# Kernel tuning notes

Measured on AMD Instinct MI355X. Metric: run time of the kernel, lower is better.

Reference implementation:

```python
import jax, jax.numpy as jnp
import numpy as np

F_DIM = 128; HID = 32; C = 8 * HID; DEPTH = 5; K = 3; HEADS = 8
JK_H = (7 * C) // 2  # 896, PyG JumpingKnowledge('lstm', C, jk_depth=7)
FLEX = 512; CLASSES = 10; GATE_H = 21 * HID
BS = 512; NPG = 23; N_NODES = BS * NPG
EPS = 1e-5


def _bn(x, gamma=None, beta=None):
    # training-mode BatchNorm1d (biased variance), affine optional
    mu = x.mean(0)
    var = x.var(0)
    y = (x - mu) * jax.lax.rsqrt(var + EPS)
    return y * gamma + beta if gamma is not None else y


def _lstm(seq, w_ih, w_hh, b_ih, b_hh):
    # seq: [T, N, C] -> hidden states [T, N, H]; torch gate order i,f,g,o
    n = seq.shape[1]
    hdim = w_hh.shape[1]
    def step(carry, xt):
        h, c = carry
        z = xt @ w_ih.T + h @ w_hh.T + b_ih + b_hh
        i, f, g, o = jnp.split(z, 4, axis=-1)
        c = jax.nn.sigmoid(f) * c + jax.nn.sigmoid(i) * jnp.tanh(g)
        h = jax.nn.sigmoid(o) * jnp.tanh(c)
        return (h, c), h
    init = (jnp.zeros((n, hdim), seq.dtype), jnp.zeros((n, hdim), seq.dtype))
    _, hs = jax.lax.scan(step, init, seq)
    return hs


def _forward(x, conv1_w, conv1_b, bn1_g, bn1_b, ll1_w, ll1_b, tag_w, tag_b,
             gat_w, gat_asrc, gat_adst, gat_b,
             lw_ih_f, lw_hh_f, lb_ih_f, lb_hh_f, lw_ih_b, lw_hh_b, lb_ih_b, lb_hh_b,
             jk_w, jk_b, fff_w1, fff_b1, fff_w2, fff_b2,
             gate_w1, gate_b1, gate_w2, gate_b2,
             conv2_w, conv2_b, bn2_g, bn2_b, fc_w, fc_b,
             edge_index, batch, num_graphs):
    n, f = x.shape
    bs = num_graphs
    # --- temporal preprocessing: PE over node axis (d_model=23), Conv1d, BN ---
    xt = x.reshape(bs, NPG, f).transpose(0, 2, 1)            # [bs, F, 23]
    pos = jnp.arange(f, dtype=x.dtype)[:, None]
    div = jnp.exp(jnp.arange(0, NPG, 2, dtype=x.dtype) * (-np.log(10000.0) / NPG))
    pe = jnp.zeros((f, NPG), x.dtype)
    pe = pe.at[:, 0::2].set(jnp.sin(pos * div))
    pe = pe.at[:, 1::2].set(jnp.cos(pos * div)[:, :(NPG - 1) // 2])
    xt = (xt + pe[None]).transpose(0, 2, 1)                  # [bs, 23, F]
    xt = jax.lax.conv_general_dilated(xt, conv1_w, (1,), [(1, 1)],
            dimension_numbers=('NCH', 'OIH', 'NCH')) + conv1_b[None, :, None]
    h = _bn(xt.reshape(n, f), bn1_g, bn1_b) @ ll1_w + ll1_b  # [N, HID]
    # --- symmetric gcn_norm (no self loops) shared by all TAGConv layers ---
    src, dst = edge_index[0], edge_index[1]
    deg = jax.ops.segment_sum(jnp.ones(src.shape, h.dtype), dst, n)
    dinv = jnp.where(deg > 0, jax.lax.rsqrt(jnp.maximum(deg, 1.0)), 0.0)
    wnorm = dinv[src] * dinv[dst]                            # [E]
    # GAT uses self loops
    loop = jnp.arange(n, dtype=src.dtype)
    src_sl = jnp.concatenate([src, loop])
    dst_sl = jnp.concatenate([dst, loop])

    jk_seq = []
    for i in range(DEPTH):
        # TAGConv: concat powers of normalized adjacency, then linear
        xs = h
        feats = [h]
        for _ in range(K):
            xs = jax.ops.segment_sum(wnorm[:, None] * xs[src], dst, n)
            feats.append(xs)
        tag = jnp.concatenate(feats, axis=-1) @ tag_w[i] + tag_b[i]
        h = _bn(h + tag)                                     # SublayerConnection (BN affine=False)
        # GATConv, heads=8, concat
        g = (h @ gat_w[i]).reshape(n, HEADS, HID)
        a = jax.nn.leaky_relu((g * gat_asrc[i]).sum(-1)[src_sl]
                              + (g * gat_adst[i]).sum(-1)[dst_sl], 0.2)  # [E', heads]
        m = jax.lax.stop_gradient(jax.ops.segment_max(a, dst_sl, n))
        ea = jnp.exp(a - m[dst_sl])
        alpha = ea / jax.ops.segment_sum(ea, dst_sl, n)[dst_sl]
        out = jax.ops.segment_sum(alpha[:, :, None] * g[src_sl], dst_sl, n)
        jk_seq.append(out.reshape(n, C) + gat_b[i])

    # JumpingKnowledge 'lstm': bi-LSTM attention over the DEPTH layer outputs
    seq = jnp.stack(jk_seq, axis=0)                          # [T=5, N, C]
    hf = _lstm(seq, lw_ih_f, lw_hh_f, lb_ih_f, lb_hh_f)
    hb = _lstm(seq[::-1], lw_ih_b, lw_hh_b, lb_ih_b, lb_hh_b)[::-1]
    att = (jnp.concatenate([hf, hb], -1) @ jk_w + jk_b)[..., 0]  # [T, N]
    w_jk = jax.nn.softmax(att, axis=0)                       # softmax over layers
    xg = (seq * w_jk[:, :, None]).sum(0)                     # [N, C]
    # FinalFeedForward + residual BN (slc4)
    ff = jax.nn.elu(xg @ fff_w1 + fff_b1) @ fff_w2 + fff_b2
    xg = _bn(xg + ff)
    # GlobalAttention pooling per graph
    gate = ((xg @ gate_w1 + gate_b1) @ gate_w2 + gate_b2)[:, 0]  # [N]
    gm = jax.lax.stop_gradient(jax.ops.segment_max(gate, batch, bs))
    ge = jnp.exp(gate - gm[batch])
    gw = ge / jax.ops.segment_sum(ge, batch, bs)[batch]
    pooled = jax.ops.segment_sum(gw[:, None] * xg, batch, bs)    # [bs, C]
    # Conv1d(1->10, k=9) over channel axis, mean over out-channels, BN, classifier
    y = jax.lax.conv_general_dilated(pooled[:, None, :], conv2_w, (1,), [(4, 4)],
            dimension_numbers=('NCH', 'OIH', 'NCH')) + conv2_b[None, :, None]
    y = _bn(y.mean(axis=1), bn2_g, bn2_b)
    return jax.nn.log_softmax(y @ fc_w + fc_b, axis=1)


def setup_inputs() -> dict:
    key = jax.random.key(0)
    it = iter(jax.random.split(key, 48))
    def rn(shape, scale=0.05):
        return jax.random.normal(next(it), shape, dtype=jnp.float32) * scale
    # complete digraph (no self loops) inside each 23-node graph
    s, d = np.meshgrid(np.arange(NPG), np.arange(NPG), indexing='ij')
    mask = s != d
    s, d = s[mask], d[mask]
    off = (np.arange(BS) * NPG)[:, None]
    src = (off + s[None, :]).reshape(-1)
    dst = (off + d[None, :]).reshape(-1)
    edge_index = jnp.asarray(np.stack([src, dst]), dtype=jnp.int32)
    batch = jnp.repeat(jnp.arange(BS, dtype=jnp.int32), NPG)
    return dict(
        x=rn((N_NODES, F_DIM), 1.0),
        edge_index=edge_index, batch=batch, num_graphs=BS,
        conv1_w=rn((NPG, NPG, 3)), conv1_b=rn((NPG,)),
        bn1_g=jnp.ones((F_DIM,), jnp.float32), bn1_b=jnp.zeros((F_DIM,), jnp.float32),
        ll1_w=rn((F_DIM, HID)), ll1_b=rn((HID,)),
        tag_w=rn((DEPTH, (K + 1) * HID, HID)), tag_b=rn((DEPTH, HID)),
        gat_w=rn((DEPTH, HID, HEADS * HID)), gat_asrc=rn((DEPTH, HEADS, HID)),
        gat_adst=rn((DEPTH, HEADS, HID)), gat_b=rn((DEPTH, HEADS * HID)),
        lw_ih_f=rn((4 * JK_H, C)), lw_hh_f=rn((4 * JK_H, JK_H)),
        lb_ih_f=rn((4 * JK_H,)), lb_hh_f=rn((4 * JK_H,)),
        lw_ih_b=rn((4 * JK_H, C)), lw_hh_b=rn((4 * JK_H, JK_H)),
        lb_ih_b=rn((4 * JK_H,)), lb_hh_b=rn((4 * JK_H,)),
        jk_w=rn((2 * JK_H, 1)), jk_b=rn((1,)),
        fff_w1=rn((C, FLEX)), fff_b1=rn((FLEX,)),
        fff_w2=rn((FLEX, C)), fff_b2=rn((C,)),
        gate_w1=rn((C, GATE_H)), gate_b1=rn((GATE_H,)),
        gate_w2=rn((GATE_H, 1)), gate_b2=rn((1,)),
        conv2_w=rn((10, 1, 9)), conv2_b=rn((10,)),
        bn2_g=jnp.ones((C,), jnp.float32), bn2_b=jnp.zeros((C,), jnp.float32),
        fc_w=rn((C, CLASSES)), fc_b=rn((CLASSES,)),
    )


def reference(x, edge_index, batch, num_graphs, conv1_w, conv1_b, bn1_g, bn1_b,
              ll1_w, ll1_b, tag_w, tag_b, gat_w, gat_asrc, gat_adst, gat_b,
              lw_ih_f, lw_hh_f, lb_ih_f, lb_hh_f, lw_ih_b, lw_hh_b, lb_ih_b, lb_hh_b,
              jk_w, jk_b, fff_w1, fff_b1, fff_w2, fff_b2,
              gate_w1, gate_b1, gate_w2, gate_b2,
              conv2_w, conv2_b, bn2_g, bn2_b, fc_w, fc_b):
    return _forward(x, conv1_w, conv1_b, bn1_g, bn1_b, ll1_w, ll1_b, tag_w, tag_b,
                    gat_w, gat_asrc, gat_adst, gat_b,
                    lw_ih_f, lw_hh_f, lb_ih_f, lb_hh_f, lw_ih_b, lw_hh_b, lb_ih_b, lb_hh_b,
                    jk_w, jk_b, fff_w1, fff_b1, fff_w2, fff_b2,
                    gate_w1, gate_b1, gate_w2, gate_b2,
                    conv2_w, conv2_b, bn2_g, bn2_b, fc_w, fc_b,
                    edge_index, batch, num_graphs)
```

## Files before the change

### kernel.cpp

```cpp
#include <hip/hip_runtime.h>
#include <math.h>

#define NNODES 11776
#define NGR    512
#define NPG    23
#define FDIM   128
#define HID    32
#define CDIM   256
#define JKH    896
#define ZCOLS  3584
#define EPSBN  1e-5f

typedef long long i64;
typedef unsigned short ushort_t;
typedef __attribute__((ext_vector_type(8))) short bf16x8;
typedef __attribute__((ext_vector_type(4))) float f32x4;

__device__ __forceinline__ float sigmoidf_(float x) { return 1.f / (1.f + expf(-x)); }

__device__ __forceinline__ ushort_t f2bf(float x) {
  unsigned u = __float_as_uint(x);
  return (ushort_t)((u + 0x7fffu + ((u >> 16) & 1u)) >> 16);
}
__device__ __forceinline__ float bf2f(ushort_t b) {
  return __uint_as_float(((unsigned)b) << 16);
}

__device__ __forceinline__ void gload16(const ushort_t* g, ushort_t* l) {
  __builtin_amdgcn_global_load_lds(
      (const __attribute__((address_space(1))) void*)g,
      (__attribute__((address_space(3))) void*)l, 16, 0, 0);
}

__global__ __launch_bounds__(256) void conv1_kernel(
    const float* __restrict__ x, const float* __restrict__ w,
    const float* __restrict__ bias, float* __restrict__ out,
    float* __restrict__ stats) {
  int b = blockIdx.x;
  __shared__ float in[NPG][FDIM];
  __shared__ float wsh[NPG * NPG * 3];
  __shared__ float cs[FDIM], cq[FDIM];
  int tid = threadIdx.x;
  if (tid < FDIM) { cs[tid] = 0.f; cq[tid] = 0.f; }
  const float c0 = -2.f * logf(10000.f) / 23.f;
  for (int idx = tid; idx < NPG * FDIM; idx += 256) {
    int p = idx >> 7, f = idx & 127;
    int j = p >> 1;
    float ang = (float)f * expf(c0 * (float)j);
    float pe = (p & 1) ? cosf(ang) : sinf(ang);
    in[p][f] = x[(i64)(b * NPG + p) * FDIM + f] + pe;
  }
  for (int idx = tid; idx < NPG * NPG * 3; idx += 256) wsh[idx] = w[idx];
  __syncthreads();
  float ls = 0.f, lq = 0.f;
  int fme = tid & 127;
  for (int idx = tid; idx < NPG * FDIM; idx += 256) {
    int o = idx >> 7, f = idx & 127;
    float acc = bias[o];
    for (int i = 0; i < NPG; ++i) {
      const float* wr = &wsh[(o * NPG + i) * 3];
      float s = in[i][f] * wr[1];
      if (f > 0)   s += in[i][f - 1] * wr[0];
      if (f < 127) s += in[i][f + 1] * wr[2];
      acc += s;
    }
    out[(i64)(b * NPG + o) * FDIM + f] = acc;
    ls += acc; lq += acc * acc;
  }
  atomicAdd(&cs[fme], ls);
  atomicAdd(&cq[fme], lq);
  __syncthreads();
  if (tid < FDIM) {
    atomicAdd(&stats[tid], cs[tid]);
    atomicAdd(&stats[FDIM + tid], cq[tid]);
  }
}

__global__ __launch_bounds__(256) void col_stats(
    const float* __restrict__ X, int rows, int cols, float* __restrict__ acc) {
  int rpt = 256 / cols;
  int c = threadIdx.x % cols;
  int rsub = threadIdx.x / cols;
  float s = 0.f, q = 0.f;
  for (int r0 = blockIdx.x * rpt; r0 < rows; r0 += gridDim.x * rpt) {
    int r = r0 + rsub;
    if (r < rows) {
      float v = X[(i64)r * cols + c];
      s += v; q += v * v;
    }
  }
  __shared__ float sh[256];
  sh[threadIdx.x] = s;
  __syncthreads();
  if (threadIdx.x < cols) {
    float t = 0.f;
    for (int g = 0; g < rpt; ++g) t += sh[g * cols + c];
    atomicAdd(&acc[c], t);
  }
  __syncthreads();
  sh[threadIdx.x] = q;
  __syncthreads();
  if (threadIdx.x < cols) {
    float t = 0.f;
    for (int g = 0; g < rpt; ++g) t += sh[g * cols + c];
    atomicAdd(&acc[cols + c], t);
  }
}

__global__ void bn_norm(const float* __restrict__ X, float* __restrict__ Y,
                        const float* __restrict__ acc, int rows, int cols) {
  i64 total = (i64)rows * cols;
  i64 idx = (i64)blockIdx.x * 256 + threadIdx.x;
  i64 stride = (i64)gridDim.x * 256;
  float invR = 1.f / (float)rows;
  for (; idx < total; idx += stride) {
    int c = (int)(idx % cols);
    float mu = acc[c] * invR;
    float var = acc[cols + c] * invR - mu * mu;
    Y[idx] = (X[idx] - mu) * rsqrtf(var + EPSBN);
  }
}

__global__ __launch_bounds__(256) void fold_ll1(
    const float* __restrict__ acc, const float* __restrict__ g,
    const float* __restrict__ be, const float* __restrict__ w,
    const float* __restrict__ lb, float* __restrict__ Wp, float* __restrict__ bp) {
  int tid = threadIdx.x;
  const float invR = 1.f / (float)NNODES;
  for (int idx = tid; idx < FDIM * HID; idx += 256) {
    int k = idx >> 5;
    float mu = acc[k] * invR;
    float var = acc[FDIM + k] * invR - mu * mu;
    float scale = g[k] * rsqrtf(var + EPSBN);
    Wp[idx] = scale * w[idx];
  }
  if (tid < HID) {
    float s = lb[tid];
    for (int k = 0; k < FDIM; ++k) {
      float mu = acc[k] * invR;
      float var = acc[FDIM + k] * invR - mu * mu;
      float scale = g[k] * rsqrtf(var + EPSBN);
      s += (be[k] - mu * scale) * w[k * HID + tid];
    }
    bp[tid] = s;
  }
}

template <int BT>
__global__ __launch_bounds__(256) void sgemm(
    const float* __restrict__ A, const float* __restrict__ B, float* __restrict__ C,
    int M, int N, int K,
    const float* __restrict__ bias, const float* __restrict__ resid,
    int act, int accumulate) {
  __shared__ float As[16][128];
  __shared__ float Bs[16][128];
  int tid = threadIdx.x;
  int bm0 = blockIdx.x * 128;
  int bn0 = blockIdx.y * 128;
  int tx = tid & 15, ty = tid >> 4;
  float acc[8][8];
#pragma unroll
  for (int i = 0; i < 8; ++i)
#pragma unroll
    for (int j = 0; j < 8; ++j) acc[i][j] = 0.f;

  int ar = tid >> 2;
  int akc = (tid & 3) << 2;
  bool bfull = (bn0 + 127 < N);

  for (int k0 = 0; k0 < K; k0 += 16) {
    {
      const float* ap = A + (i64)(bm0 + ar) * K + k0 + akc;
      float4 a0 = *(const float4*)ap;
      float4 a1 = *(const float4*)(ap + (i64)64 * K);
      As[akc + 0][ar] = a0.x; As[akc + 1][ar] = a0.y;
      As[akc + 2][ar] = a0.z; As[akc + 3][ar] = a0.w;
      As[akc + 0][ar + 64] = a1.x; As[akc + 1][ar + 64] = a1.y;
      As[akc + 2][ar + 64] = a1.z; As[akc + 3][ar + 64] = a1.w;
    }
    if (BT) {
      int br = tid >> 1;
      int bkc = (tid & 1) << 3;
      const float* bp = B + (i64)(bn0 + br) * K + k0 + bkc;
      float4 b0 = *(const float4*)bp;
      float4 b1 = *(const float4*)(bp + 4);
      Bs[bkc + 0][br] = b0.x; Bs[bkc + 1][br] = b0.y;
      Bs[bkc + 2][br] = b0.z; Bs[bkc + 3][br] = b0.w;
      Bs[bkc + 4][br] = b1.x; Bs[bkc + 5][br] = b1.y;
      Bs[bkc + 6][br] = b1.z; Bs[bkc + 7][br] = b1.w;
    } else {
      int bk = tid >> 4;
      int bn = (tid & 15) << 3;
      const float* bp = B + (i64)(k0 + bk) * N + bn0 + bn;
      if (bfull) {
        *(float4*)&Bs[bk][bn] = *(const float4*)bp;
        *(float4*)&Bs[bk][bn + 4] = *(const float4*)(bp + 4);
      } else {
#pragma unroll
        for (int q = 0; q < 8; ++q)
          Bs[bk][bn + q] = (bn0 + bn + q < N) ? bp[q] : 0.f;
      }
    }
    __syncthreads();
#pragma unroll
    for (int kk = 0; kk < 16; ++kk) {
      float a[8], b[8];
      *(float4*)(a)     = *(const float4*)&As[kk][ty * 8];
      *(float4*)(a + 4) = *(const float4*)&As[kk][ty * 8 + 4];
      *(float4*)(b)     = *(const float4*)&Bs[kk][tx * 8];
      *(float4*)(b + 4) = *(const float4*)&Bs[kk][tx * 8 + 4];
#pragma unroll
      for (int i = 0; i < 8; ++i)
#pragma unroll
        for (int j = 0; j < 8; ++j)
          acc[i][j] = fmaf(a[i], b[j], acc[i][j]);
    }
    __syncthreads();
  }
#pragma unroll
  for (int i = 0; i < 8; ++i) {
    int m = bm0 + ty * 8 + i;
#pragma unroll
    for (int j = 0; j < 8; ++j) {
      int n = bn0 + tx * 8 + j;
      if (n < N) {
        i64 ci = (i64)m * N + n;
        float v = acc[i][j];
        if (accumulate) {
          C[ci] += v;
        } else {
          if (bias) v += bias[n];
          if (act == 1) v = v > 0.f ? v : expm1f(v);
          if (resid) v += resid[ci];
          C[ci] = v;
        }
      }
    }
  }
}

__global__ __launch_bounds__(256) void tag_fused(
    const float* __restrict__ hbuf, const float* __restrict__ tag_w,
    const float* __restrict__ tag_b, float* __restrict__ hres,
    float* __restrict__ stats) {
  int b = blockIdx.x, tid = threadIdx.x;
  __shared__ float fe[NPG][FDIM];
  __shared__ float wsh[FDIM * HID];
  __shared__ float S[HID];
  __shared__ float cs[HID], cq[HID];
  if (tid < HID) { cs[tid] = 0.f; cq[tid] = 0.f; }
  const float* hp = hbuf + (i64)b * NPG * HID;
  for (int idx = tid; idx < NPG * HID; idx += 256) fe[idx >> 5][idx & 31] = hp[idx];
  for (int idx = tid; idx < FDIM * HID; idx += 256) wsh[idx] = tag_w[idx];
  __syncthreads();
  if (tid < HID) {
    float s = 0.f;
    for (int p = 0; p < NPG; ++p) s += fe[p][tid];
    S[tid] = s;
  }
  __syncthreads();
  const float wn = 1.f / 22.f;
  for (int idx = tid; idx < NPG * HID; idx += 256) {
    int p = idx >> 5, c = idx & 31;
    float f0 = fe[p][c], Sc = S[c];
    float f1 = (Sc - f0) * wn;
    float f2 = (Sc - f1) * wn;
    float f3 = (Sc - f2) * wn;
    fe[p][HID + c] = f1;
    fe[p][2 * HID + c] = f2;
    fe[p][3 * HID + c] = f3;
  }
  __syncthreads();
  for (int idx = tid; idx < NPG * HID; idx += 256) {
    int p = idx >> 5, c = idx & 31;
    float acc = tag_b[c];
#pragma unroll 8
    for (int k = 0; k < FDIM; ++k) acc += fe[p][k] * wsh[k * HID + c];
    float v = fe[p][c] + acc;
    hres[(i64)(b * NPG + p) * HID + c] = v;
    atomicAdd(&cs[c], v);
    atomicAdd(&cq[c], v * v);
  }
  __syncthreads();
  if (tid < HID) {
    atomicAdd(&stats[tid], cs[tid]);
    atomicAdd(&stats[HID + tid], cq[tid]);
  }
}

__global__ __launch_bounds__(256) void gat_fused(
    const float* __restrict__ hres, const float* __restrict__ stats,
    const float* __restrict__ gat_w, const float* __restrict__ asrc,
    const float* __restrict__ adst, const float* __restrict__ gbias,
    float* __restrict__ hout, ushort_t* __restrict__ outseq) {
  int b = blockIdx.x, tid = threadIdx.x;
  __shared__ float hn[NPG * HID];
  __shared__ float gsh[NPG * CDIM];
  __shared__ float ssrc[NPG * 8], sdst[NPG * 8], sinv[NPG * 8];
  __shared__ float ealpha[NPG * NPG * 8];
  const float invR = 1.f / (float)NNODES;
  for (int idx = tid; idx < NPG * HID; idx += 256) {
    int c = idx & 31;
    float mu = stats[c] * invR;
    float var = stats[HID + c] * invR - mu * mu;
    float v = (hres[(i64)b * NPG * HID + idx] - mu) * rsqrtf(var + EPSBN);
    hn[idx] = v;
    hout[(i64)b * NPG * HID + idx] = v;
  }
  __syncthreads();
  for (int idx = tid; idx < NPG * CDIM; idx += 256) {
    int p = idx >> 8, d = idx & 255;
    float acc = 0.f;
#pragma unroll
    for (int k = 0; k < HID; ++k) acc += hn[p * HID + k] * gat_w[k * CDIM + d];
    gsh[idx] = acc;
  }
  __syncthreads();
  if (tid < NPG * 8) {
    int p = tid >> 3, hd = tid & 7;
    float s1 = 0.f, s2 = 0.f;
    const float* gp = &gsh[p * CDIM + hd * 32];
#pragma unroll
    for (int d = 0; d < 32; ++d) {
      s1 += gp[d] * asrc[hd * 32 + d];
      s2 += gp[d] * adst[hd * 32 + d];
    }
    ssrc[tid] = s1;
    sdst[tid] = s2;
  }
  __syncthreads();
  if (tid < NPG * 8) {
    int v = tid >> 3, hd = tid & 7;
    float sd = sdst[v * 8 + hd];
    float e[NPG];
    float m = -1e30f;
#pragma unroll
    for (int u = 0; u < NPG; ++u) {
      float xv = ssrc[u * 8 + hd] + sd;
      xv = xv > 0.f ? xv : 0.2f * xv;
      e[u] = xv;
      m = fmaxf(m, xv);
    }
    float s = 0.f;
#pragma unroll
    for (int u = 0; u < NPG; ++u) {
      float t = expf(e[u] - m);
      ealpha[(v * NPG + u) * 8 + hd] = t;
      s += t;
    }
    sinv[tid] = 1.f / s;
  }
  __syncthreads();
  {
    int hd = tid >> 5, d = tid & 31;
    const i64 base = (i64)b * NPG * CDIM;
    for (int v = 0; v < NPG; ++v) {
      float acc = 0.f;
#pragma unroll
      for (int u = 0; u < NPG; ++u)
        acc += ealpha[(v * NPG + u) * 8 + hd] * gsh[u * CDIM + hd * 32 + d];
      outseq[base + (i64)v * CDIM + hd * 32 + d] =
          f2bf(acc * sinv[v * 8 + hd] + gbias[hd * 32 + d]);
    }
  }
}

__global__ void pack_w(const float* __restrict__ w, ushort_t* __restrict__ wp,
                       int ldK) {
  i64 total = (i64)ZCOLS * ldK;
  i64 idx = (i64)blockIdx.x * 256 + threadIdx.x;
  i64 stride = (i64)gridDim.x * 256;
  for (; idx < total; idx += stride) {
    int r = (int)(idx / ldK), k = (int)(idx % ldK);
    int g = r / JKH, jj = r % JKH;
    int p = (jj >> 4) * 64 + g * 16 + (jj & 15);
    wp[(i64)p * ldK + k] = f2bf(w[idx]);
  }
}

__global__ void pack_b(const float* __restrict__ a, const float* __restrict__ b,
                       float* __restrict__ bp) {
  int r = blockIdx.x * 256 + threadIdx.x;
  if (r < ZCOLS) {
    int g = r / JKH, jj = r % JKH;
    int p = (jj >> 4) * 64 + g * 16 + (jj & 15);
    bp[p] = a[r] + b[r];
  }
}

template <int HASH>
__global__ __launch_bounds__(256) void lstm_step(
    const ushort_t* __restrict__ Aseq,
    const ushort_t* __restrict__ Wih,
    const ushort_t* __restrict__ Hprev,
    const ushort_t* __restrict__ Whh,
    const float*  __restrict__ bspk,
    float* __restrict__ Cst,
    ushort_t* __restrict__ Hout,
    const float* __restrict__ jkw,
    float* __restrict__ attp) {
  __shared__ ushort_t As[128 * 64];
  __shared__ ushort_t Bs[128 * 64];
  int tid = threadIdx.x;
  int w = tid >> 6, lane = tid & 63;
  int m0 = blockIdx.x * 128;
  int n0 = blockIdx.y * 128;
  f32x4 acc[4][4];
#pragma unroll
  for (int a = 0; a < 4; ++a)
#pragma unroll
    for (int b = 0; b < 4; ++b) acc[a][b] = (f32x4){0.f, 0.f, 0.f, 0.f};

  const ushort_t* aptr = Aseq;
  const ushort_t* bptr = Wih;
  int lda = CDIM, K = CDIM;
  for (int phase = 0; phase < (HASH ? 2 : 1); ++phase) {
    for (int k0 = 0; k0 < K; k0 += 64) {
#pragma unroll
      for (int i = 0; i < 4; ++i) {
        int r = w + i * 4;
        int s = r * 64 + lane;
        int row = s >> 3;
        int kc = (s & 7) ^ (row & 7);
        gload16(aptr + (i64)(m0 + row) * lda + k0 + kc * 8, &As[r * 512]);
        gload16(bptr + (i64)(n0 + row) * lda + k0 + kc * 8, &Bs[r * 512]);
      }
      __syncthreads();
#pragma unroll
      for (int ks = 0; ks < 2; ++ks) {
        bf16x8 af[4], bfr[4];
        int kq = ks * 4 + (lane >> 4);
#pragma unroll
        for (int mi = 0; mi < 4; ++mi) {
          int row = (w & 1) * 64 + mi * 16 + (lane & 15);
          int pos = row * 8 + (kq ^ (row & 7));
          af[mi] = *(const bf16x8*)&As[pos * 8];
        }
#pragma unroll
        for (int ni = 0; ni < 4; ++ni) {
          int row = (w >> 1) * 64 + ni * 16 + (lane & 15);
          int pos = row * 8 + (kq ^ (row & 7));
          bfr[ni] = *(const bf16x8*)&Bs[pos * 8];
        }
#pragma unroll
        for (int mi = 0; mi < 4; ++mi)
#pragma unroll
          for (int ni = 0; ni < 4; ++ni)
            acc[mi][ni] = __builtin_amdgcn_mfma_f32_16x16x32_bf16(
                af[mi], bfr[ni], acc[mi][ni], 0, 0, 0);
      }
      __syncthreads();
    }
    aptr = Hprev; bptr = Whh; lda = JKH; K = JKH;
  }

  int jb = (n0 >> 6) + (w >> 1);
  int j = jb * 16 + (lane & 15);
  float jw = jkw[j];
  float bsi = bspk[jb * 64 + (lane & 15)];
  float bsf = bspk[jb * 64 + 16 + (lane & 15)];
  float bsg = bspk[jb * 64 + 32 + (lane & 15)];
  float bso = bspk[jb * 64 + 48 + (lane & 15)];
#pragma unroll
  for (int mi = 0; mi < 4; ++mi) {
#pragma unroll
    for (int reg = 0; reg < 4; ++reg) {
      int m = m0 + (w & 1) * 64 + mi * 16 + (lane >> 4) * 4 + reg;
      float zi = acc[mi][0][reg] + bsi;
      float zf = acc[mi][1][reg] + bsf;
      float zg = acc[mi][2][reg] + bsg;
      float zo = acc[mi][3][reg] + bso;
      i64 ci = (i64)m * JKH + j;
      float cv = sigmoidf_(zi) * tanhf(zg);
      if (HASH) cv += sigmoidf_(zf) * Cst[ci];
      Cst[ci] = cv;
      float hv = sigmoidf_(zo) * tanhf(cv);
      Hout[ci] = f2bf(hv);
      float av = hv * jw;
      av += __shfl_xor(av, 1, 64);
      av += __shfl_xor(av, 2, 64);
      av += __shfl_xor(av, 4, 64);
      av += __shfl_xor(av, 8, 64);
      if ((lane & 15) == 0) atomicAdd(&attp[m], av);
    }
  }
}

__global__ __launch_bounds__(256) void jk_combine(const float* __restrict__ att,
                                                  const ushort_t* __restrict__ seq,
                                                  float* __restrict__ xg) {
  int n = blockIdx.x, c = threadIdx.x;
  float a[5];
  float m = -1e30f;
#pragma unroll
  for (int t = 0; t < 5; ++t) {
    a[t] = att[(i64)t * NNODES + n] + att[(i64)(5 + t) * NNODES + n];
    m = fmaxf(m, a[t]);
  }
  float s = 0.f;
#pragma unroll
  for (int t = 0; t < 5; ++t) { a[t] = expf(a[t] - m); s += a[t]; }
  float inv = 1.f / s;
  float acc = 0.f;
#pragma unroll
  for (int t = 0; t < 5; ++t)
    acc += bf2f(seq[((i64)t * NNODES + n) * CDIM + c]) * (a[t] * inv);
  xg[(i64)n * CDIM + c] = acc;
}

__global__ void fill0(float* __restrict__ p, i64 nfloat) {
  i64 i = (i64)blockIdx.x * 256 + threadIdx.x;
  i64 stride = (i64)gridDim.x * 256;
  for (; i < nfloat; i += stride) p[i] = 0.f;
}

__global__ __launch_bounds__(256) void fold_gate(
    const float* __restrict__ w1, const float* __restrict__ b1,
    const float* __restrict__ w2, const float* __restrict__ b2,
    float* __restrict__ v, float* __restrict__ b0) {
  int tid = threadIdx.x;
  float s = 0.f;
  for (int j = 0; j < 672; ++j) s += w1[tid * 672 + j] * w2[j];
  v[tid] = s;
  float p = 0.f;
  for (int j = tid; j < 672; j += 256) p += b1[j] * w2[j];
  __shared__ float sh[4];
#pragma unroll
  for (int o = 32; o > 0; o >>= 1) p += __shfl_down(p, o, 64);
  if ((tid & 63) == 0) sh[tid >> 6] = p;
  __syncthreads();
  if (tid == 0) b0[0] = sh[0] + sh[1] + sh[2] + sh[3] + b2[0];
}

__global__ __launch_bounds__(256) void pool_kernel(
    const float* __restrict__ xgn, const float* __restrict__ v,
    const float* __restrict__ b0, float* __restrict__ pooled) {
  int g = blockIdx.x, tid = threadIdx.x;
  __shared__ float gw[NPG];
  __shared__ float sh[4];
  float myv = v[tid];
  for (int p = 0; p < NPG; ++p) {
    float val = xgn[(i64)(g * NPG + p) * CDIM + tid] * myv;
#pragma unroll
    for (int o = 32; o > 0; o >>= 1) val += __shfl_down(val, o, 64);
    if ((tid & 63) == 0) sh[tid >> 6] = val;
    __syncthreads();
    if (tid == 0) gw[p] = sh[0] + sh[1] + sh[2] + sh[3] + b0[0];
    __syncthreads();
  }
  if (tid == 0) {
    float m = -1e30f;
    for (int p = 0; p < NPG; ++p) m = fmaxf(m, gw[p]);
    float s = 0.f;
    for (int p = 0; p < NPG; ++p) { gw[p] = expf(gw[p] - m); s += gw[p]; }
    float inv = 1.f / s;
    for (int p = 0; p < NPG; ++p) gw[p] *= inv;
  }
  __syncthreads();
  float acc = 0.f;
  for (int p = 0; p < NPG; ++p)
    acc += gw[p] * xgn[(i64)(g * NPG + p) * CDIM + tid];
  pooled[(i64)g * CDIM + tid] = acc;
}

__global__ void fold_conv2(const float* __restrict__ w, const float* __restrict__ b,
                           float* __restrict__ wbar) {
  int tid = threadIdx.x;
  if (tid < 9) {
    float s = 0.f;
    for (int o = 0; o < 10; ++o) s += w[o * 9 + tid];
    wbar[tid] = s * 0.1f;
  } else if (tid == 9) {
    float s = 0.f;
    for (int o = 0; o < 10; ++o) s += b[o];
    wbar[9] = s * 0.1f;
  }
}

__global__ __launch_bounds__(256) void conv2mean(const float* __restrict__ pooled,
                                                 const float* __restrict__ wbar,
                                                 float* __restrict__ y2) {
  int b = blockIdx.x, h = threadIdx.x;
  __shared__ float row[CDIM];
  row[h] = pooled[(i64)b * CDIM + h];
  __syncthreads();
  float s = wbar[9];
#pragma unroll
  for (int t = 0; t < 9; ++t) {
    int hh = h + t - 4;
    if (hh >= 0 && hh < CDIM) s += row[hh] * wbar[t];
  }
  y2[(i64)b * CDIM + h] = s;
}

__global__ __launch_bounds__(256) void final_fc(
    const float* __restrict__ y2, const float* __restrict__ acc,
    const float* __restrict__ g2, const float* __restrict__ b2,
    const float* __restrict__ fcw, const float* __restrict__ fcb,
    float* __restrict__ out) {
  int b = blockIdx.x, tid = threadIdx.x;
  __shared__ float yn[CDIM];
  __shared__ float logits[10];
  __shared__ float red[2];
  float mu = acc[tid] / 512.f;
  float var = acc[CDIM + tid] / 512.f - mu * mu;
  yn[tid] = (y2[(i64)b * CDIM + tid] - mu) * rsqrtf(var + EPSBN) * g2[tid] + b2[tid];
  __syncthreads();
  if (tid < 10) {
    float s = fcb[tid];
    for (int h = 0; h < CDIM; ++h) s += yn[h] * fcw[h * 10 + tid];
    logits[tid] = s;
  }
  __syncthreads();
  if (tid == 0) {
    float m = -1e30f;
    for (int o = 0; o < 10; ++o) m = fmaxf(m, logits[o]);
    float s = 0.f;
    for (int o = 0; o < 10; ++o) s += expf(logits[o] - m);
    red[0] = m;
    red[1] = logf(s);
  }
  __syncthreads();
  if (tid < 10) out[(i64)b * 10 + tid] = logits[tid] - red[0] - red[1];
}

extern "C" void kernel_launch(void* const* d_in, const int* in_sizes, int n_in,
                              void* d_out, int out_size, void* d_ws, size_t ws_size,
                              hipStream_t stream) {
  (void)in_sizes; (void)n_in; (void)out_size;
  const float* x        = (const float*)d_in[0];
  const float* conv1_w  = (const float*)d_in[4];
  const float* conv1_b  = (const float*)d_in[5];
  const float* bn1_g    = (const float*)d_in[6];
  const float* bn1_b    = (const float*)d_in[7];
  const float* ll1_w    = (const float*)d_in[8];
  const float* ll1_b    = (const float*)d_in[9];
  const float* tag_w    = (const float*)d_in[10];
  const float* tag_b    = (const float*)d_in[11];
  const float* gat_w    = (const float*)d_in[12];
  const float* gat_asrc = (const float*)d_in[13];
  const float* gat_adst = (const float*)d_in[14];
  const float* gat_b    = (const float*)d_in[15];
  const float* lw_ih[2] = {(const float*)d_in[16], (const float*)d_in[20]};
  const float* lw_hh[2] = {(const float*)d_in[17], (const float*)d_in[21]};
  const float* lb_ih[2] = {(const float*)d_in[18], (const float*)d_in[22]};
  const float* lb_hh[2] = {(const float*)d_in[19], (const float*)d_in[23]};
  const float* jk_w     = (const float*)d_in[24];
  const float* fff_w1   = (const float*)d_in[26];
  const float* fff_b1   = (const float*)d_in[27];
  const float* fff_w2   = (const float*)d_in[28];
  const float* fff_b2   = (const float*)d_in[29];
  const float* gate_w1  = (const float*)d_in[30];
  const float* gate_b1  = (const float*)d_in[31];
  const float* gate_w2  = (const float*)d_in[32];
  const float* gate_b2  = (const float*)d_in[33];
  const float* conv2_w  = (const float*)d_in[34];
  const float* conv2_b  = (const float*)d_in[35];
  const float* bn2_g    = (const float*)d_in[36];
  const float* bn2_b    = (const float*)d_in[37];
  const float* fc_w     = (const float*)d_in[38];
  const float* fc_b     = (const float*)d_in[39];
  float* out = (float*)d_out;

  float* ws = (float*)d_ws;
  i64 off = 0;
  auto alloc = [&](i64 n) { float* p = ws + off; off += (n + 15) & ~(i64)15; return p; };
  ushort_t* seqb = (ushort_t*)alloc(7536640);
  float* att = alloc(10 * NNODES);
  float* st1 = alloc(256);
  float* st2 = alloc(5 * 64);
  float* st4 = alloc(512);
  float* st5 = alloc(512);
  i64 zcount = 117760 + 256 + 320 + 512 + 512 + 80;
  float* xg     = alloc((i64)NNODES * CDIM);
  float* hbuf   = alloc((i64)NNODES * HID);
  float* hres   = alloc((i64)NNODES * HID);
  float* Wp     = alloc(FDIM * HID);
  float* bp     = alloc(64);
  ushort_t* wihb[2]; ushort_t* whhb[2]; float* bspk[2];
  for (int d = 0; d < 2; ++d) {
    wihb[d] = (ushort_t*)alloc((i64)ZCOLS * CDIM / 2);
    whhb[d] = (ushort_t*)alloc((i64)ZCOLS * JKH / 2);
    bspk[d] = alloc(ZCOLS);
  }
  float* gatev  = alloc(CDIM);
  float* gateb0 = alloc(16);
  float* wbar   = alloc(16);
  float* pooled = alloc((i64)NGR * CDIM);
  float* y2     = alloc((i64)NGR * CDIM);
  float* Zs = ws + off;
  i64 S = (i64)(ws_size / 4) - off;
  if (S < 0) S = 0;

  int Tch = (int)(S / 172032); if (Tch < 1) Tch = 1; if (Tch > 92) Tch = 92;
  i64 Sff = S - 6029312;
  int Tf = (int)(Sff / 65536); if (Tf < 1) Tf = 1; if (Tf > 92) Tf = 92;

  float* xconv = Zs;
  ushort_t* hA = (ushort_t*)Zs;
  ushort_t* hB = hA + (i64)Tch * 128 * JKH;
  float* cch   = (float*)(hB + (i64)Tch * 128 * JKH);
  float* s4  = Zs;
  float* xgn = s4 + 3014656;
  float* ff1 = xgn + 3014656;

  fill0<<<512, 256, 0, stream>>>(att, zcount);
  for (int d = 0; d < 2; ++d) {
    pack_w<<<2048, 256, 0, stream>>>(lw_ih[d], wihb[d], CDIM);
    pack_w<<<4096, 256, 0, stream>>>(lw_hh[d], whhb[d], JKH);
    pack_b<<<14, 256, 0, stream>>>(lb_ih[d], lb_hh[d], bspk[d]);
  }

  conv1_kernel<<<NGR, 256, 0, stream>>>(x, conv1_w, conv1_b, xconv, st1);
  fold_ll1<<<1, 256, 0, stream>>>(st1, bn1_g, bn1_b, ll1_w, ll1_b, Wp, bp);
  sgemm<0><<<dim3(92, 1), 256, 0, stream>>>(xconv, Wp, hbuf, NNODES, HID, FDIM,
                                            bp, nullptr, 0, 0);

  for (int i = 0; i < 5; ++i) {
    tag_fused<<<NGR, 256, 0, stream>>>(hbuf, tag_w + (i64)i * FDIM * HID,
                                       tag_b + i * HID, hres, st2 + i * 64);
    gat_fused<<<NGR, 256, 0, stream>>>(hres, st2 + i * 64,
                                       gat_w + (i64)i * HID * CDIM,
                                       gat_asrc + i * 256, gat_adst + i * 256,
                                       gat_b + i * 256, hbuf,
                                       seqb + (i64)i * NNODES * CDIM);
  }

  for (int dir = 0; dir < 2; ++dir) {
    for (int t0 = 0; t0 < 92; t0 += Tch) {
      int tiles = (92 - t0 < Tch) ? (92 - t0) : Tch;
      i64 r0 = (i64)t0 * 128;
      ushort_t* hp[2] = {hA, hB};
      for (int t = 0; t < 5; ++t) {
        int ts = dir ? 4 - t : t;
        const ushort_t* Ax = seqb + ((i64)ts * NNODES + r0) * CDIM;
        float* attp = att + (i64)(dir * 5 + ts) * NNODES + r0;
        if (t == 0)
          lstm_step<0><<<dim3(tiles, 28), 256, 0, stream>>>(
              Ax, wihb[dir], nullptr, nullptr, bspk[dir], cch, hp[0],
              jk_w + dir * JKH, attp);
        else
          lstm_step<1><<<dim3(tiles, 28), 256, 0, stream>>>(
              Ax, wihb[dir], hp[(t + 1) & 1], whhb[dir], bspk[dir], cch, hp[t & 1],
              jk_w + dir * JKH, attp);
      }
    }
  }
  jk_combine<<<NNODES, 256, 0, stream>>>(att, seqb, xg);

  for (int t0 = 0; t0 < 92; t0 += Tf) {
    int tiles = (92 - t0 < Tf) ? (92 - t0) : Tf;
    int rows = tiles * 128;
    i64 r0 = (i64)t0 * 128;
    sgemm<0><<<dim3(tiles, 4), 256, 0, stream>>>(xg + r0 * CDIM, fff_w1, ff1,
                                                 rows, 512, CDIM, fff_b1, nullptr, 1, 0);
    sgemm<0><<<dim3(tiles, 2), 256, 0, stream>>>(ff1, fff_w2, s4 + r0 * CDIM,
                                                 rows, CDIM, 512, fff_b2,
                                                 xg + r0 * CDIM, 0, 0);
  }
  col_stats<<<184, 256, 0, stream>>>(s4, NNODES, CDIM, st4);
  bn_norm<<<4096, 256, 0, stream>>>(s4, xgn, st4, NNODES, CDIM);

  fold_gate<<<1, 256, 0, stream>>>(gate_w1, gate_b1, gate_w2, gate_b2, gatev, gateb0);
  pool_kernel<<<NGR, 256, 0, stream>>>(xgn, gatev, gateb0, pooled);
  fold_conv2<<<1, 64, 0, stream>>>(conv2_w, conv2_b, wbar);
  conv2mean<<<NGR, 256, 0, stream>>>(pooled, wbar, y2);
  col_stats<<<64, 256, 0, stream>>>(y2, NGR, CDIM, st5);
  final_fc<<<NGR, 256, 0, stream>>>(y2, st5, bn2_g, bn2_b, fc_w, fc_b, out);
}
```

Measured before the change: 1.898 ms.

## Use bf16 MFMA for feed-forward GEMMs, fuse TAG into GAT, batch LSTM attention atomics

The two feed-forward GEMMs move from fp32 sgemm to a bf16 MFMA GEMM. This needs transposed bf16 weight packs and a bf16 copy of the JK output, and the intermediate activation is stored in bf16. The next layer's TAG computation is fused into the tail of the GAT kernel, so each layer needs one launch and one fewer global round-trip of the hidden state. LSTM attention partial sums are first reduced in shared memory, so each block issues one global atomic per row instead of many. The bf16 GEMMs lower precision, and the fused kernel uses more shared memory.

```diff
diff --git a/kernel.cpp b/kernel.cpp
--- a/kernel.cpp
+++ b/kernel.cpp
@@ -288,24 +288,26 @@
   }
 }
 
-__global__ __launch_bounds__(256) void gat_fused(
+__global__ __launch_bounds__(256) void gat_tag_fused(
     const float* __restrict__ hres, const float* __restrict__ stats,
     const float* __restrict__ gat_w, const float* __restrict__ asrc,
     const float* __restrict__ adst, const float* __restrict__ gbias,
-    float* __restrict__ hout, ushort_t* __restrict__ outseq) {
+    ushort_t* __restrict__ outseq,
+    const float* __restrict__ tag_w_next, const float* __restrict__ tag_b_next,
+    float* __restrict__ hres_out, float* __restrict__ stats_next, int has_next) {
   int b = blockIdx.x, tid = threadIdx.x;
   __shared__ float hn[NPG * HID];
-  __shared__ float gsh[NPG * CDIM];
   __shared__ float ssrc[NPG * 8], sdst[NPG * 8], sinv[NPG * 8];
-  __shared__ float ealpha[NPG * NPG * 8];
+  __shared__ float buf[10120];
+  __shared__ float S[HID], cs[HID], cq[HID];
+  float* gsh = buf;
+  float* ealpha = buf + 5888;
   const float invR = 1.f / (float)NNODES;
   for (int idx = tid; idx < NPG * HID; idx += 256) {
     int c = idx & 31;
     float mu = stats[c] * invR;
     float var = stats[HID + c] * invR - mu * mu;
-    float v = (hres[(i64)b * NPG * HID + idx] - mu) * rsqrtf(var + EPSBN);
-    hn[idx] = v;
-    hout[(i64)b * NPG * HID + idx] = v;
+    hn[idx] = (hres[(i64)b * NPG * HID + idx] - mu) * rsqrtf(var + EPSBN);
   }
   __syncthreads();
   for (int idx = tid; idx < NPG * CDIM; idx += 256) {
@@ -362,6 +364,48 @@
       outseq[base + (i64)v * CDIM + hd * 32 + d] =
           f2bf(acc * sinv[v * 8 + hd] + gbias[hd * 32 + d]);
     }
+  }
+  if (!has_next) return;
+  __syncthreads();
+  float* fe = buf;
+  float* wsh = buf + 2944;
+  if (tid < HID) { cs[tid] = 0.f; cq[tid] = 0.f; }
+  for (int idx = tid; idx < FDIM * HID; idx += 256) wsh[idx] = tag_w_next[idx];
+  for (int idx = tid; idx < NPG * HID; idx += 256)
+    fe[(idx >> 5) * FDIM + (idx & 31)] = hn[idx];
+  __syncthreads();
+  if (tid < HID) {
+    float s = 0.f;
+    for (int p = 0; p < NPG; ++p) s += fe[p * FDIM + tid];
+    S[tid] = s;
+  }
+  __syncthreads();
+  const float wn = 1.f / 22.f;
+  for (int idx = tid; idx < NPG * HID; idx += 256) {
+    int p = idx >> 5, c = idx & 31;
+    float f0 = fe[p * FDIM + c], Sc = S[c];
+    float f1 = (Sc - f0) * wn;
+    float f2 = (Sc - f1) * wn;
+    float f3 = (Sc - f2) * wn;
+    fe[p * FDIM + HID + c] = f1;
+    fe[p * FDIM + 2 * HID + c] = f2;
+    fe[p * FDIM + 3 * HID + c] = f3;
+  }
+  __syncthreads();
+  for (int idx = tid; idx < NPG * HID; idx += 256) {
+    int p = idx >> 5, c = idx & 31;
+    float acc = tag_b_next[c];
+#pragma unroll 8
+    for (int k = 0; k < FDIM; ++k) acc += fe[p * FDIM + k] * wsh[k * HID + c];
+    float v = fe[p * FDIM + c] + acc;
+    hres_out[(i64)(b * NPG + p) * HID + c] = v;
+    atomicAdd(&cs[c], v);
+    atomicAdd(&cq[c], v * v);
+  }
+  __syncthreads();
+  if (tid < HID) {
+    atomicAdd(&stats_next[tid], cs[tid]);
+    atomicAdd(&stats_next[HID + tid], cq[tid]);
   }
 }
 
@@ -385,6 +429,17 @@
     int g = r / JKH, jj = r % JKH;
     int p = (jj >> 4) * 64 + g * 16 + (jj & 15);
     bp[p] = a[r] + b[r];
+  }
+}
+
+__global__ void pack_t(const float* __restrict__ w, ushort_t* __restrict__ wt,
+                       int K, int N) {
+  i64 total = (i64)K * N;
+  i64 idx = (i64)blockIdx.x * 256 + threadIdx.x;
+  i64 stride = (i64)gridDim.x * 256;
+  for (; idx < total; idx += stride) {
+    int k = (int)(idx / N), n = (int)(idx % N);
+    wt[(i64)n * K + k] = f2bf(w[idx]);
   }
 }
 
@@ -401,6 +456,7 @@
     float* __restrict__ attp) {
   __shared__ ushort_t As[128 * 64];
   __shared__ ushort_t Bs[128 * 64];
+  __shared__ float att_s[128];
   int tid = threadIdx.x;
   int w = tid >> 6, lane = tid & 63;
   int m0 = blockIdx.x * 128;
@@ -454,6 +510,9 @@
     aptr = Hprev; bptr = Whh; lda = JKH; K = JKH;
   }
 
+  if (tid < 128) att_s[tid] = 0.f;
+  __syncthreads();
+
   int jb = (n0 >> 6) + (w >> 1);
   int j = jb * 16 + (lane & 15);
   float jw = jkw[j];
@@ -465,7 +524,8 @@
   for (int mi = 0; mi < 4; ++mi) {
 #pragma unroll
     for (int reg = 0; reg < 4; ++reg) {
-      int m = m0 + (w & 1) * 64 + mi * 16 + (lane >> 4) * 4 + reg;
+      int mloc = (w & 1) * 64 + mi * 16 + (lane >> 4) * 4 + reg;
+      int m = m0 + mloc;
       float zi = acc[mi][0][reg] + bsi;
       float zf = acc[mi][1][reg] + bsf;
       float zg = acc[mi][2][reg] + bsg;
@@ -481,14 +541,89 @@
       av += __shfl_xor(av, 2, 64);
       av += __shfl_xor(av, 4, 64);
       av += __shfl_xor(av, 8, 64);
-      if ((lane & 15) == 0) atomicAdd(&attp[m], av);
+      if ((lane & 15) == 0) atomicAdd(&att_s[mloc], av);
+    }
+  }
+  __syncthreads();
+  if (tid < 128) atomicAdd(&attp[m0 + tid], att_s[tid]);
+}
+
+template <int ACT, int BF16OUT>
+__global__ __launch_bounds__(256) void mfma_gemm(
+    const ushort_t* __restrict__ A, const ushort_t* __restrict__ Bt, int K,
+    const float* __restrict__ bias, const float* __restrict__ resid,
+    float* __restrict__ Cf, ushort_t* __restrict__ Cb, int N) {
+  __shared__ ushort_t As[128 * 64];
+  __shared__ ushort_t Bs[128 * 64];
+  int tid = threadIdx.x;
+  int w = tid >> 6, lane = tid & 63;
+  int m0 = blockIdx.x * 128;
+  int n0 = blockIdx.y * 128;
+  f32x4 acc[4][4];
+#pragma unroll
+  for (int a = 0; a < 4; ++a)
+#pragma unroll
+    for (int b = 0; b < 4; ++b) acc[a][b] = (f32x4){0.f, 0.f, 0.f, 0.f};
+
+  for (int k0 = 0; k0 < K; k0 += 64) {
+#pragma unroll
+    for (int i = 0; i < 4; ++i) {
+      int r = w + i * 4;
+      int s = r * 64 + lane;
+      int row = s >> 3;
+      int kc = (s & 7) ^ (row & 7);
+      gload16(A + (i64)(m0 + row) * K + k0 + kc * 8, &As[r * 512]);
+      gload16(Bt + (i64)(n0 + row) * K + k0 + kc * 8, &Bs[r * 512]);
+    }
+    __syncthreads();
+#pragma unroll
+    for (int ks = 0; ks < 2; ++ks) {
+      bf16x8 af[4], bfr[4];
+      int kq = ks * 4 + (lane >> 4);
+#pragma unroll
+      for (int mi = 0; mi < 4; ++mi) {
+        int row = (w & 1) * 64 + mi * 16 + (lane & 15);
+        int pos = row * 8 + (kq ^ (row & 7));
+        af[mi] = *(const bf16x8*)&As[pos * 8];
+      }
+#pragma unroll
+      for (int ni = 0; ni < 4; ++ni) {
+        int row = (w >> 1) * 64 + ni * 16 + (lane & 15);
+        int pos = row * 8 + (kq ^ (row & 7));
+        bfr[ni] = *(const bf16x8*)&Bs[pos * 8];
+      }
+#pragma unroll
+      for (int mi = 0; mi < 4; ++mi)
+#pragma unroll
+        for (int ni = 0; ni < 4; ++ni)
+          acc[mi][ni] = __builtin_amdgcn_mfma_f32_16x16x32_bf16(
+              af[mi], bfr[ni], acc[mi][ni], 0, 0, 0);
+    }
+    __syncthreads();
+  }
+#pragma unroll
+  for (int ni = 0; ni < 4; ++ni) {
+    int n = n0 + (w >> 1) * 64 + ni * 16 + (lane & 15);
+    float bv = bias[n];
+#pragma unroll
+    for (int mi = 0; mi < 4; ++mi) {
+#pragma unroll
+      for (int reg = 0; reg < 4; ++reg) {
+        int m = m0 + (w & 1) * 64 + mi * 16 + (lane >> 4) * 4 + reg;
+        float v = acc[mi][ni][reg] + bv;
+        if (ACT) v = v > 0.f ? v : expm1f(v);
+        i64 ci = (i64)m * N + n;
+        if (BF16OUT) Cb[ci] = f2bf(v);
+        else Cf[ci] = v + resid[ci];
+      }
     }
   }
 }
 
 __global__ __launch_bounds__(256) void jk_combine(const float* __restrict__ att,
                                                   const ushort_t* __restrict__ seq,
-                                                  float* __restrict__ xg) {
+                                                  float* __restrict__ xg,
+                                                  ushort_t* __restrict__ xgb) {
   int n = blockIdx.x, c = threadIdx.x;
   float a[5];
   float m = -1e30f;
@@ -506,6 +641,7 @@
   for (int t = 0; t < 5; ++t)
     acc += bf2f(seq[((i64)t * NNODES + n) * CDIM + c]) * (a[t] * inv);
   xg[(i64)n * CDIM + c] = acc;
+  xgb[(i64)n * CDIM + c] = f2bf(acc);
 }
 
 __global__ void fill0(float* __restrict__ p, i64 nfloat) {
@@ -668,11 +804,12 @@
   ushort_t* seqb = (ushort_t*)alloc(7536640);
   float* att = alloc(10 * NNODES);
   float* st1 = alloc(256);
-  float* st2 = alloc(5 * 64);
+  float* st2 = alloc(6 * 64);
   float* st4 = alloc(512);
   float* st5 = alloc(512);
-  i64 zcount = 117760 + 256 + 320 + 512 + 512 + 80;
+  i64 zcount = (i64)(st5 - att) + 512;
   float* xg     = alloc((i64)NNODES * CDIM);
+  ushort_t* xgb = (ushort_t*)alloc((i64)NNODES * CDIM / 2);
   float* hbuf   = alloc((i64)NNODES * HID);
   float* hres   = alloc((i64)NNODES * HID);
   float* Wp     = alloc(FDIM * HID);
@@ -683,6 +820,8 @@
     whhb[d] = (ushort_t*)alloc((i64)ZCOLS * JKH / 2);
     bspk[d] = alloc(ZCOLS);
   }
+  ushort_t* w1t = (ushort_t*)alloc(512 * 256 / 2);
+  ushort_t* w2t = (ushort_t*)alloc(256 * 512 / 2);
   float* gatev  = alloc(CDIM);
   float* gateb0 = alloc(16);
   float* wbar   = alloc(16);
@@ -694,7 +833,7 @@
 
   int Tch = (int)(S / 172032); if (Tch < 1) Tch = 1; if (Tch > 92) Tch = 92;
   i64 Sff = S - 6029312;
-  int Tf = (int)(Sff / 65536); if (Tf < 1) Tf = 1; if (Tf > 92) Tf = 92;
+  int Tf = (int)(Sff / 32768); if (Tf < 1) Tf = 1; if (Tf > 92) Tf = 92;
 
   float* xconv = Zs;
   ushort_t* hA = (ushort_t*)Zs;
@@ -702,7 +841,7 @@
   float* cch   = (float*)(hB + (i64)Tch * 128 * JKH);
   float* s4  = Zs;
   float* xgn = s4 + 3014656;
-  float* ff1 = xgn + 3014656;
+  ushort_t* ff1b = (ushort_t*)(xgn + 3014656);
 
   fill0<<<512, 256, 0, stream>>>(att, zcount);
   for (int d = 0; d < 2; ++d) {
@@ -710,20 +849,23 @@
     pack_w<<<4096, 256, 0, stream>>>(lw_hh[d], whhb[d], JKH);
     pack_b<<<14, 256, 0, stream>>>(lb_ih[d], lb_hh[d], bspk[d]);
   }
+  pack_t<<<512, 256, 0, stream>>>(fff_w1, w1t, CDIM, 512);
+  pack_t<<<512, 256, 0, stream>>>(fff_w2, w2t, 512, CDIM);
 
   conv1_kernel<<<NGR, 256, 0, stream>>>(x, conv1_w, conv1_b, xconv, st1);
   fold_ll1<<<1, 256, 0, stream>>>(st1, bn1_g, bn1_b, ll1_w, ll1_b, Wp, bp);
   sgemm<0><<<dim3(92, 1), 256, 0, stream>>>(xconv, Wp, hbuf, NNODES, HID, FDIM,
                                             bp, nullptr, 0, 0);
 
+  tag_fused<<<NGR, 256, 0, stream>>>(hbuf, tag_w, tag_b, hres, st2);
   for (int i = 0; i < 5; ++i) {
-    tag_fused<<<NGR, 256, 0, stream>>>(hbuf, tag_w + (i64)i * FDIM * HID,
-                                       tag_b + i * HID, hres, st2 + i * 64);
-    gat_fused<<<NGR, 256, 0, stream>>>(hres, st2 + i * 64,
-                                       gat_w + (i64)i * HID * CDIM,
-                                       gat_asrc + i * 256, gat_adst + i * 256,
-                                       gat_b + i * 256, hbuf,
-                                       seqb + (i64)i * NNODES * CDIM);
+    int nx = (i < 4) ? (i + 1) : 0;
+    gat_tag_fused<<<NGR, 256, 0, stream>>>(
+        hres, st2 + i * 64, gat_w + (i64)i * HID * CDIM,
+        gat_asrc + i * 256, gat_adst + i * 256, gat_b + i * 256,
+        seqb + (i64)i * NNODES * CDIM,
+        tag_w + (i64)nx * FDIM * HID, tag_b + nx * HID,
+        hres, st2 + (i + 1) * 64, (i < 4) ? 1 : 0);
   }
 
   for (int dir = 0; dir < 2; ++dir) {
@@ -746,17 +888,15 @@
       }
     }
   }
-  jk_combine<<<NNODES, 256, 0, stream>>>(att, seqb, xg);
+  jk_combine<<<NNODES, 256, 0, stream>>>(att, seqb, xg, xgb);
 
   for (int t0 = 0; t0 < 92; t0 += Tf) {
     int tiles = (92 - t0 < Tf) ? (92 - t0) : Tf;
-    int rows = tiles * 128;
     i64 r0 = (i64)t0 * 128;
-    sgemm<0><<<dim3(tiles, 4), 256, 0, stream>>>(xg + r0 * CDIM, fff_w1, ff1,
-                                                 rows, 512, CDIM, fff_b1, nullptr, 1, 0);
-    sgemm<0><<<dim3(tiles, 2), 256, 0, stream>>>(ff1, fff_w2, s4 + r0 * CDIM,
-                                                 rows, CDIM, 512, fff_b2,
-                                                 xg + r0 * CDIM, 0, 0);
+    mfma_gemm<1, 1><<<dim3(tiles, 4), 256, 0, stream>>>(
+        xgb + r0 * CDIM, w1t, CDIM, fff_b1, nullptr, nullptr, ff1b, 512);
+    mfma_gemm<0, 0><<<dim3(tiles, 2), 256, 0, stream>>>(
+        ff1b, w2t, 512, fff_b2, xg + r0 * CDIM, s4 + r0 * CDIM, nullptr, CDIM);
   }
   col_stats<<<184, 256, 0, stream>>>(s4, NNODES, CDIM, st4);
   bn_norm<<<4096, 256, 0, stream>>>(s4, xgn, st4, NNODES, CDIM);
```

Measured after the change: 1.763 ms. -7.1%, faster.
